# Kernel optimization log

Hardware: AMD Instinct MI355X
Metric: run time of the kernel (lower is better)

The kernel has to match this reference:

```python
import jax, jax.numpy as jnp
import numpy as np

B, NG, H, G, T0, T1 = 4096, 3000, 6, 30, 500, 50  # batch, genes, hidden, genes/term, leaf terms, mid terms
EPS = 1e-5  # BatchNorm1d default eps


def _bn(x, gamma, beta):
    # training-mode BatchNorm1d: biased batch stats over the batch axis
    m = x.mean(axis=0)
    v = ((x - m) ** 2).mean(axis=0)
    return gamma * (x - m) / jnp.sqrt(v + EPS) + beta


def setup_inputs() -> dict:
    key = jax.random.key(0)
    ks = iter(jax.random.split(key, 32))
    rn = lambda shape, s=0.05: jax.random.normal(next(ks), shape, dtype=jnp.float32) * s
    return dict(
        cell_features=jax.random.normal(next(ks), (B, NG), dtype=jnp.float32),
        Wdg=rn((T0 + T1 + 1, G, NG)), bdg=rn((T0 + T1 + 1, G)),
        W0=rn((T0, H, G)), b0=rn((T0, H)), gam0=jnp.ones((T0, H), jnp.float32), bet0=jnp.zeros((T0, H), jnp.float32),
        aw0=rn((T0, H)), ab0=rn((T0,)), av0=rn((T0,)), ac0=rn((T0,)),
        W1=rn((T1, H, 10 * H + G)), b1=rn((T1, H)), gam1=jnp.ones((T1, H), jnp.float32), bet1=jnp.zeros((T1, H), jnp.float32),
        aw1=rn((T1, H)), ab1=rn((T1,)), av1=rn((T1,)), ac1=rn((T1,)),
        W2=rn((H, T1 * H + G)), b2=rn((H,)), gam2=jnp.ones((H,), jnp.float32), bet2=jnp.zeros((H,), jnp.float32),
        aw2=rn((H,)), ab2=rn(()), av2=rn(()), ac2=rn(()),
    )


def reference(cell_features, Wdg, bdg,
              W0, b0, gam0, bet0, aw0, ab0, av0, ac0,
              W1, b1, gam1, bet1, aw1, ab1, av1, ac1,
              W2, b2, gam2, bet2, aw2, ab2, av2, ac2):
    # direct_gene_layer for every term: Linear(ngene -> genes_per_term), no activation
    dg = jnp.einsum('bn,tgn->btg', cell_features, Wdg) + bdg  # [B, 551, G]
    # ---- layer 0 (leaves): input = direct gene output only ----
    z0 = jnp.tanh(jnp.einsum('btg,thg->bth', dg[:, :T0], W0) + b0)
    n0 = _bn(z0, gam0, bet0)                                   # [B, T0, H]
    aux0 = jnp.tanh(jnp.einsum('bth,th->bt', n0, aw0) + ab0) * av0 + ac0
    # ---- layer 1: term t's children are leaves [10t, 10t+10); concat children + direct genes ----
    in1 = jnp.concatenate([n0.reshape(B, T1, 10 * H), dg[:, T0:T0 + T1]], axis=-1)  # [B, T1, 90]
    z1 = jnp.tanh(jnp.einsum('bti,thi->bth', in1, W1) + b1)
    n1 = _bn(z1, gam1, bet1)                                   # [B, T1, H]
    aux1 = jnp.tanh(jnp.einsum('bth,th->bt', n1, aw1) + ab1) * av1 + ac1
    # ---- root: children = all mid terms + direct genes ----
    in2 = jnp.concatenate([n1.reshape(B, T1 * H), dg[:, -1]], axis=-1)  # [B, 330]
    z2 = jnp.tanh(in2 @ W2.T + b2)
    n2 = _bn(z2, gam2, bet2)                                   # [B, H]
    aux2 = jnp.tanh(n2 @ aw2 + ab2) * av2 + ac2                # [B]
    # flatten (aux_out_map, term_NN_out_map) into one array for a single comparable output
    aux_all = jnp.concatenate([aux0, aux1, aux2[:, None]], axis=1)              # [B, 551]
    nn_all = jnp.concatenate([n0.reshape(B, -1), n1.reshape(B, -1), n2], axis=1)  # [B, 551*H]
    return jnp.concatenate([aux_all, nn_all], axis=1)          # [B, 3857]
```

## Files before the change

kernel.cpp:

```cpp
#include <hip/hip_runtime.h>
#include <hip/hip_bf16.h>

#define BATCH 4096
#define NGENE 3000
#define HID   6
#define GPT   30
#define T0N   500
#define T1N   50
#define KP    3008
#define MROWS 4608
#define OUTW  3857
#define BNEPS 1e-5f

typedef __attribute__((ext_vector_type(8))) __bf16 bf16x8;
typedef __attribute__((ext_vector_type(4))) float f32x4;
typedef __attribute__((ext_vector_type(8))) unsigned short ushort8;

__device__ __forceinline__ unsigned short f2bf(float f) {
  unsigned int u = __builtin_bit_cast(unsigned int, f);
  u = (u + 0x7fffu + ((u >> 16) & 1u)) >> 16;
  return (unsigned short)u;
}

__device__ __forceinline__ void gload_lds16(const void* g, void* l) {
  __builtin_amdgcn_global_load_lds(
      (const __attribute__((address_space(1))) unsigned int*)g,
      (__attribute__((address_space(3))) unsigned int*)l, 16, 0, 0);
}

__global__ void cast_cell(const float* __restrict__ x, ushort8* __restrict__ y) {
  int idx = blockIdx.x * 256 + threadIdx.x;
  int r = idx / 376, c8 = idx - r * 376;
  int c = c8 * 8;
  ushort8 o = (ushort8)0;
  if (c < NGENE) {
    const float4* p = (const float4*)(x + (size_t)r * NGENE + c);
    float4 a = p[0], b = p[1];
    o[0] = f2bf(a.x); o[1] = f2bf(a.y); o[2] = f2bf(a.z); o[3] = f2bf(a.w);
    o[4] = f2bf(b.x); o[5] = f2bf(b.y); o[6] = f2bf(b.z); o[7] = f2bf(b.w);
  }
  y[idx] = o;
}

__global__ void v0_build(const float* __restrict__ Wdg, const float* __restrict__ W0,
                         unsigned short* __restrict__ abuf) {
  int n = blockIdx.x * 256 + threadIdx.x;
  int t = blockIdx.y;
  if (n >= KP) return;
  bool valid = n < NGENE;
  float x[GPT];
#pragma unroll
  for (int g = 0; g < GPT; ++g)
    x[g] = valid ? Wdg[((size_t)(t * GPT + g)) * NGENE + n] : 0.f;
#pragma unroll
  for (int h = 0; h < HID; ++h) {
    const float* w = W0 + (t * HID + h) * GPT;
    float s = 0.f;
#pragma unroll
    for (int g = 0; g < GPT; ++g) s += x[g] * w[g];
    abuf[((size_t)(t * HID + h)) * KP + n] = valid ? f2bf(s) : (unsigned short)0;
  }
}

__global__ void cast_wdg_mid(const float* __restrict__ w, ushort8* __restrict__ y) {
  int idx = blockIdx.x * 256 + threadIdx.x;
  if (idx >= 1530 * 376) return;
  int r = idx / 376, c8 = idx - r * 376;
  int c = c8 * 8;
  ushort8 o = (ushort8)0;
  if (c < NGENE) {
    const float4* p = (const float4*)(w + (size_t)(15000 + r) * NGENE + c);
    float4 a = p[0], b = p[1];
    o[0] = f2bf(a.x); o[1] = f2bf(a.y); o[2] = f2bf(a.z); o[3] = f2bf(a.w);
    o[4] = f2bf(b.x); o[5] = f2bf(b.y); o[6] = f2bf(b.z); o[7] = f2bf(b.w);
  }
  y[(size_t)(3000 + r) * 376 + c8] = o;
}

__global__ void zero_tail(ushort8* __restrict__ y) {
  int idx = blockIdx.x * 256 + threadIdx.x;
  if (idx < 78 * 376) y[(size_t)4530 * 376 + idx] = (ushort8)0;
}

__global__ void build_bias(const float* __restrict__ bdg, const float* __restrict__ W0,
                           const float* __restrict__ b0, float* __restrict__ bias) {
  int idx = blockIdx.x * 256 + threadIdx.x;
  if (idx >= MROWS) return;
  float v = 0.f;
  if (idx < 3000) {
    int t = idx / HID;
    float s = b0[idx];
#pragma unroll
    for (int g = 0; g < GPT; ++g) s += W0[idx * GPT + g] * bdg[t * GPT + g];
    v = s;
  } else if (idx < 4530) {
    v = bdg[15000 + idx - 3000];
  }
  bias[idx] = v;
}

__global__ __launch_bounds__(256) void gemm_fused(
    const unsigned short* __restrict__ A,
    const unsigned short* __restrict__ Bt,
    const float* __restrict__ bias,
    float* __restrict__ C) {
  __shared__ unsigned short smem[8192];
  const int tid  = threadIdx.x;
  const int wave = tid >> 6, lane = tid & 63;
  const int wm = wave >> 1, wn = wave & 1;
  const int quad = lane >> 4, fr = lane & 15;
  const int m0 = blockIdx.y * 128, n0 = blockIdx.x * 128;
  const int lrow = lane >> 2;
  const int lcol = (lane & 3) * 8;

  f32x4 acc[16] = {};

  for (int kt = 0; kt < KP / 32; ++kt) {
    const int k0 = kt * 32;
#pragma unroll
    for (int q = 0; q < 4; ++q) {
      int chunk = q * 4 + wave;
      const unsigned short* gsrc;
      if (chunk < 8) {
        int row = m0 + chunk * 16 + lrow;
        gsrc = A + (size_t)row * KP + k0 + lcol;
      } else {
        int row = n0 + (chunk - 8) * 16 + lrow;
        gsrc = Bt + (size_t)row * KP + k0 + lcol;
      }
      gload_lds16(gsrc, &smem[chunk * 512]);
    }
    asm volatile("s_waitcnt vmcnt(0)" ::: "memory");
    __syncthreads();

    bf16x8 af[4], bfr[4];
#pragma unroll
    for (int tm = 0; tm < 4; ++tm)
      af[tm] = ((const bf16x8*)smem)[((wm * 64 + tm * 16 + fr) * 32 + quad * 8) >> 3];
#pragma unroll
    for (int tn = 0; tn < 4; ++tn)
      bfr[tn] = ((const bf16x8*)smem)[(4096 + (wn * 64 + tn * 16 + fr) * 32 + quad * 8) >> 3];
#pragma unroll
    for (int tm = 0; tm < 4; ++tm)
#pragma unroll
      for (int tn = 0; tn < 4; ++tn)
        acc[tm * 4 + tn] = __builtin_amdgcn_mfma_f32_16x16x32_bf16(
            af[tm], bfr[tn], acc[tm * 4 + tn], 0, 0, 0);
    __syncthreads();
  }

#pragma unroll
  for (int tm = 0; tm < 4; ++tm) {
#pragma unroll
    for (int tn = 0; tn < 4; ++tn) {
      int n = n0 + wn * 64 + tn * 16 + fr;
#pragma unroll
      for (int r = 0; r < 4; ++r) {
        int m = m0 + wm * 64 + tm * 16 + quad * 4 + r;
        float v = acc[tm * 4 + tn][r] + bias[m];
        if (m < 3000) v = tanhf(v);
        C[(size_t)m * BATCH + n] = v;
      }
    }
  }
}

__global__ void colstatsT(const float* __restrict__ zT, float* __restrict__ st, int ncols) {
  int c = blockIdx.x;
  if (c >= ncols) return;
  const float* p = zT + (size_t)c * BATCH;
  float s = 0.f, q = 0.f;
  for (int i = threadIdx.x; i < BATCH; i += 256) {
    float v = p[i];
    s += v; q += v * v;
  }
#pragma unroll
  for (int off = 32; off > 0; off >>= 1) {
    s += __shfl_down(s, off);
    q += __shfl_down(q, off);
  }
  __shared__ float ls[8];
  int lane = threadIdx.x & 63, w = threadIdx.x >> 6;
  if (lane == 0) { ls[2 * w] = s; ls[2 * w + 1] = q; }
  __syncthreads();
  if (threadIdx.x == 0) {
    st[2 * c]     = ls[0] + ls[2] + ls[4] + ls[6];
    st[2 * c + 1] = ls[1] + ls[3] + ls[5] + ls[7];
  }
}

__global__ void bnfin(const float* __restrict__ st, const float* __restrict__ gam,
                      const float* __restrict__ bet, float* __restrict__ ss, int ncols) {
  int c = blockIdx.x * 256 + threadIdx.x;
  if (c >= ncols) return;
  float m = st[2 * c] * (1.f / BATCH);
  float v = st[2 * c + 1] * (1.f / BATCH) - m * m;
  float sc = gam[c] * rsqrtf(v + BNEPS);
  ss[2 * c] = sc;
  ss[2 * c + 1] = bet[c] - m * sc;
}

__global__ void norm_emit(const float* __restrict__ zT, const float* __restrict__ ss,
                          float* __restrict__ out, int ncols, int outoff) {
  __shared__ float tile[64][65];
  int lane = threadIdx.x & 63, w = threadIdx.x >> 6;
  int c0 = blockIdx.x * 64, b0 = blockIdx.y * 64;
#pragma unroll
  for (int i = 0; i < 16; ++i) {
    int cc = w * 16 + i, c = c0 + cc;
    float n = 0.f;
    if (c < ncols)
      n = zT[(size_t)c * BATCH + b0 + lane] * ss[2 * c] + ss[2 * c + 1];
    tile[cc][lane] = n;
  }
  __syncthreads();
  int c = c0 + lane;
  if (c < ncols) {
#pragma unroll
    for (int i = 0; i < 16; ++i) {
      int rr = w * 16 + i;
      out[(size_t)(b0 + rr) * OUTW + outoff + c] = tile[lane][rr];
    }
  }
}

__global__ void aux_head(const float* __restrict__ zT, const float* __restrict__ ss,
                         const float* __restrict__ aw, const float* __restrict__ ab,
                         const float* __restrict__ av, const float* __restrict__ ac,
                         float* __restrict__ out, int nterm, int auxoff) {
  int lane = threadIdx.x & 63, tg = threadIdx.x >> 6;
  int t = blockIdx.x * 4 + tg;
  if (t >= nterm) return;
  int b = blockIdx.y * 64 + lane;
  float s = ab[t];
#pragma unroll
  for (int h = 0; h < HID; ++h) {
    int c = t * HID + h;
    float n = zT[(size_t)c * BATCH + b] * ss[2 * c] + ss[2 * c + 1];
    s += n * aw[c];
  }
  out[(size_t)b * OUTW + auxoff + t] = tanhf(s) * av[t] + ac[t];
}

__global__ void layer1_zT(const float* __restrict__ C, const float* __restrict__ ss0,
                          const float* __restrict__ W1, const float* __restrict__ b1,
                          float* __restrict__ z1T, float* __restrict__ st) {
  int lane = threadIdx.x & 63, tg = threadIdx.x >> 6;
  int t = blockIdx.x * 4 + tg;
  if (t >= T1N) return;
  int b = blockIdx.y * 64 + lane;
  const float* z0T = C;
  const float* dgm = C + (size_t)3000 * BATCH;
  float x[90];
#pragma unroll
  for (int j = 0; j < 60; ++j) {
    int c = t * 60 + j;
    x[j] = z0T[(size_t)c * BATCH + b] * ss0[2 * c] + ss0[2 * c + 1];
  }
#pragma unroll
  for (int g = 0; g < GPT; ++g)
    x[60 + g] = dgm[(size_t)(t * GPT + g) * BATCH + b];
#pragma unroll
  for (int h = 0; h < HID; ++h) {
    int c = t * HID + h;
    const float* w = W1 + c * 90;
    float s = b1[c];
#pragma unroll
    for (int i = 0; i < 90; ++i) s += x[i] * w[i];
    float z = tanhf(s);
    z1T[(size_t)c * BATCH + b] = z;
    float s1 = z, s2 = z * z;
#pragma unroll
    for (int off = 32; off > 0; off >>= 1) {
      s1 += __shfl_down(s1, off);
      s2 += __shfl_down(s2, off);
    }
    if (lane == 0) {
      atomicAdd(&st[2 * c], s1);
      atomicAdd(&st[2 * c + 1], s2);
    }
  }
}

__global__ void root_zT(const float* __restrict__ C, const float* __restrict__ z1T,
                        const float* __restrict__ ss1, const float* __restrict__ W2,
                        const float* __restrict__ b2, float* __restrict__ z2T,
                        float* __restrict__ st) {
  int b = blockIdx.x * 256 + threadIdx.x;
  int lane = threadIdx.x & 63;
  const float* dgr = C + (size_t)4500 * BATCH;
  float s[HID];
#pragma unroll
  for (int h = 0; h < HID; ++h) s[h] = b2[h];
  for (int c = 0; c < 300; ++c) {
    float n = z1T[(size_t)c * BATCH + b] * ss1[2 * c] + ss1[2 * c + 1];
#pragma unroll
    for (int h = 0; h < HID; ++h) s[h] += n * W2[h * 330 + c];
  }
#pragma unroll
  for (int g = 0; g < GPT; ++g) {
    float d = dgr[(size_t)g * BATCH + b];
#pragma unroll
    for (int h = 0; h < HID; ++h) s[h] += d * W2[h * 330 + 300 + g];
  }
#pragma unroll
  for (int h = 0; h < HID; ++h) {
    float z = tanhf(s[h]);
    z2T[(size_t)h * BATCH + b] = z;
    float s1 = z, s2 = z * z;
#pragma unroll
    for (int off = 32; off > 0; off >>= 1) {
      s1 += __shfl_down(s1, off);
      s2 += __shfl_down(s2, off);
    }
    if (lane == 0) {
      atomicAdd(&st[2 * h], s1);
      atomicAdd(&st[2 * h + 1], s2);
    }
  }
}

__global__ void root_emit(const float* __restrict__ z2T, const float* __restrict__ ss2,
                          const float* __restrict__ aw2, const float* __restrict__ ab2,
                          const float* __restrict__ av2, const float* __restrict__ ac2,
                          float* __restrict__ out) {
  int b = blockIdx.x * 256 + threadIdx.x;
  float s = ab2[0];
#pragma unroll
  for (int h = 0; h < HID; ++h) {
    float n = z2T[(size_t)h * BATCH + b] * ss2[2 * h] + ss2[2 * h + 1];
    out[(size_t)b * OUTW + 3851 + h] = n;
    s += n * aw2[h];
  }
  out[(size_t)b * OUTW + 550] = tanhf(s) * av2[0] + ac2[0];
}

extern "C" void kernel_launch(void* const* d_in, const int* in_sizes, int n_in,
                              void* d_out, int out_size, void* d_ws, size_t ws_size,
                              hipStream_t stream) {
  (void)in_sizes; (void)n_in; (void)out_size; (void)ws_size;
  const float* cell = (const float*)d_in[0];
  const float* Wdg  = (const float*)d_in[1];
  const float* bdg  = (const float*)d_in[2];
  const float* W0   = (const float*)d_in[3];
  const float* b0   = (const float*)d_in[4];
  const float* gam0 = (const float*)d_in[5];
  const float* bet0 = (const float*)d_in[6];
  const float* aw0  = (const float*)d_in[7];
  const float* ab0  = (const float*)d_in[8];
  const float* av0  = (const float*)d_in[9];
  const float* ac0  = (const float*)d_in[10];
  const float* W1   = (const float*)d_in[11];
  const float* b1   = (const float*)d_in[12];
  const float* gam1 = (const float*)d_in[13];
  const float* bet1 = (const float*)d_in[14];
  const float* aw1  = (const float*)d_in[15];
  const float* ab1  = (const float*)d_in[16];
  const float* av1  = (const float*)d_in[17];
  const float* ac1  = (const float*)d_in[18];
  const float* W2   = (const float*)d_in[19];
  const float* b2   = (const float*)d_in[20];
  const float* gam2 = (const float*)d_in[21];
  const float* bet2 = (const float*)d_in[22];
  const float* aw2  = (const float*)d_in[23];
  const float* ab2  = (const float*)d_in[24];
  const float* av2  = (const float*)d_in[25];
  const float* ac2  = (const float*)d_in[26];
  float* out = (float*)d_out;

  char* ws = (char*)d_ws;
  unsigned short* cellb = (unsigned short*)(ws);
  unsigned short* abuf  = (unsigned short*)(ws + 24641536);
  float*          C     = (float*)(ws + 52363264);
  float*          z1T   = (float*)(ws + 127860736);
  float*          z2T   = (float*)(ws + 132775936);
  float*          st    = (float*)(ws + 132874240);
  float*          ssb   = (float*)(ws + 132907008);
  float*          bias  = (float*)(ws + 132939776);
  float* st0 = st,  *st1 = st + 2 * 3000,  *st2 = st + 2 * 3300;
  float* ss0 = ssb, *ss1 = ssb + 2 * 3000, *ss2 = ssb + 2 * 3300;

  hipMemsetAsync(st, 0, 32768, stream);
  cast_cell<<<6016, 256, 0, stream>>>(cell, (ushort8*)cellb);
  v0_build<<<dim3(12, T0N), 256, 0, stream>>>(Wdg, W0, abuf);
  cast_wdg_mid<<<2248, 256, 0, stream>>>(Wdg, (ushort8*)abuf);
  zero_tail<<<115, 256, 0, stream>>>((ushort8*)abuf);
  build_bias<<<18, 256, 0, stream>>>(bdg, W0, b0, bias);

  gemm_fused<<<dim3(32, 36), 256, 0, stream>>>(abuf, cellb, bias, C);

  colstatsT<<<3000, 256, 0, stream>>>(C, st0, 3000);
  bnfin<<<12, 256, 0, stream>>>(st0, gam0, bet0, ss0, 3000);
  norm_emit<<<dim3(47, 64), 256, 0, stream>>>(C, ss0, out, 3000, 551);
  aux_head<<<dim3(125, 64), 256, 0, stream>>>(C, ss0, aw0, ab0, av0, ac0, out, 500, 0);

  layer1_zT<<<dim3(13, 64), 256, 0, stream>>>(C, ss0, W1, b1, z1T, st1);
  bnfin<<<2, 256, 0, stream>>>(st1, gam1, bet1, ss1, 300);
  norm_emit<<<dim3(5, 64), 256, 0, stream>>>(z1T, ss1, out, 300, 3551);
  aux_head<<<dim3(13, 64), 256, 0, stream>>>(z1T, ss1, aw1, ab1, av1, ac1, out, 50, 500);

  root_zT<<<16, 256, 0, stream>>>(C, z1T, ss1, W2, b2, z2T, st2);
  bnfin<<<1, 256, 0, stream>>>(st2, gam2, bet2, ss2, 6);
  root_emit<<<16, 256, 0, stream>>>(z2T, ss2, aw2, ab2, av2, ac2, out);
}
```

Before: 693.2 us.

## Pipeline GEMM with triple-buffered LDS, fuse BN stats, merge prep and aux kernels

The GEMM moves to 256x128 tiles with 512 threads, triple-buffered LDS prefetch two k-steps ahead, an XOR swizzle for LDS reads, a remapped block order, and s_setprio around the MFMAs. Column sums and sums of squares are now reduced in the GEMM epilogue with atomics, which removes the separate colstats pass over C. The small prep kernels (cast, mid-weight cast, zero tail, bias) are merged into one launch, and norm_emit is fused with aux_head so the tile already in LDS feeds the aux outputs. The trade-offs are atomic contention, different float summation order in the statistics, and higher register and LDS pressure.

```diff
diff --git a/kernel.cpp b/kernel.cpp
--- a/kernel.cpp
+++ b/kernel.cpp
@@ -11,6 +11,8 @@
 #define MROWS 4608
 #define OUTW  3857
 #define BNEPS 1e-5f
+#define NIT   94
+#define BUFU  12288
 
 typedef __attribute__((ext_vector_type(8))) __bf16 bf16x8;
 typedef __attribute__((ext_vector_type(4))) float f32x4;
@@ -28,18 +30,52 @@
       (__attribute__((address_space(3))) unsigned int*)l, 16, 0, 0);
 }
 
-__global__ void cast_cell(const float* __restrict__ x, ushort8* __restrict__ y) {
-  int idx = blockIdx.x * 256 + threadIdx.x;
-  int r = idx / 376, c8 = idx - r * 376;
-  int c = c8 * 8;
-  ushort8 o = (ushort8)0;
-  if (c < NGENE) {
-    const float4* p = (const float4*)(x + (size_t)r * NGENE + c);
-    float4 a = p[0], b = p[1];
-    o[0] = f2bf(a.x); o[1] = f2bf(a.y); o[2] = f2bf(a.z); o[3] = f2bf(a.w);
-    o[4] = f2bf(b.x); o[5] = f2bf(b.y); o[6] = f2bf(b.z); o[7] = f2bf(b.w);
-  }
-  y[idx] = o;
+__global__ void prep(const float* __restrict__ cell, const float* __restrict__ Wdg,
+                     const float* __restrict__ bdg, const float* __restrict__ W0,
+                     const float* __restrict__ b0,
+                     ushort8* __restrict__ cellb, ushort8* __restrict__ abuf8,
+                     float* __restrict__ bias) {
+  int blk = blockIdx.x;
+  if (blk < 6016) {
+    int idx = blk * 256 + threadIdx.x;
+    int r = idx / 376, c8 = idx - r * 376;
+    int c = c8 * 8;
+    ushort8 o = (ushort8)0;
+    if (c < NGENE) {
+      const float4* p = (const float4*)(cell + (size_t)r * NGENE + c);
+      float4 a = p[0], b = p[1];
+      o[0] = f2bf(a.x); o[1] = f2bf(a.y); o[2] = f2bf(a.z); o[3] = f2bf(a.w);
+      o[4] = f2bf(b.x); o[5] = f2bf(b.y); o[6] = f2bf(b.z); o[7] = f2bf(b.w);
+    }
+    cellb[idx] = o;
+  } else if (blk < 8378) {
+    int idx = (blk - 6016) * 256 + threadIdx.x;
+    if (idx >= 1608 * 376) return;
+    int r = idx / 376, c8 = idx - r * 376;
+    int c = c8 * 8;
+    ushort8 o = (ushort8)0;
+    if (r < 1530 && c < NGENE) {
+      const float4* p = (const float4*)(Wdg + (size_t)(15000 + r) * NGENE + c);
+      float4 a = p[0], b = p[1];
+      o[0] = f2bf(a.x); o[1] = f2bf(a.y); o[2] = f2bf(a.z); o[3] = f2bf(a.w);
+      o[4] = f2bf(b.x); o[5] = f2bf(b.y); o[6] = f2bf(b.z); o[7] = f2bf(b.w);
+    }
+    abuf8[(size_t)(3000 + r) * 376 + c8] = o;
+  } else {
+    int idx = (blk - 8378) * 256 + threadIdx.x;
+    if (idx >= MROWS) return;
+    float v = 0.f;
+    if (idx < 3000) {
+      int t = idx / HID;
+      float s = b0[idx];
+#pragma unroll
+      for (int g = 0; g < GPT; ++g) s += W0[idx * GPT + g] * bdg[t * GPT + g];
+      v = s;
+    } else if (idx < 4530) {
+      v = bdg[15000 + idx - 3000];
+    }
+    bias[idx] = v;
+  }
 }
 
 __global__ void v0_build(const float* __restrict__ Wdg, const float* __restrict__ W0,
@@ -62,130 +98,106 @@
   }
 }
 
-__global__ void cast_wdg_mid(const float* __restrict__ w, ushort8* __restrict__ y) {
-  int idx = blockIdx.x * 256 + threadIdx.x;
-  if (idx >= 1530 * 376) return;
-  int r = idx / 376, c8 = idx - r * 376;
-  int c = c8 * 8;
-  ushort8 o = (ushort8)0;
-  if (c < NGENE) {
-    const float4* p = (const float4*)(w + (size_t)(15000 + r) * NGENE + c);
-    float4 a = p[0], b = p[1];
-    o[0] = f2bf(a.x); o[1] = f2bf(a.y); o[2] = f2bf(a.z); o[3] = f2bf(a.w);
-    o[4] = f2bf(b.x); o[5] = f2bf(b.y); o[6] = f2bf(b.z); o[7] = f2bf(b.w);
-  }
-  y[(size_t)(3000 + r) * 376 + c8] = o;
-}
-
-__global__ void zero_tail(ushort8* __restrict__ y) {
-  int idx = blockIdx.x * 256 + threadIdx.x;
-  if (idx < 78 * 376) y[(size_t)4530 * 376 + idx] = (ushort8)0;
-}
-
-__global__ void build_bias(const float* __restrict__ bdg, const float* __restrict__ W0,
-                           const float* __restrict__ b0, float* __restrict__ bias) {
-  int idx = blockIdx.x * 256 + threadIdx.x;
-  if (idx >= MROWS) return;
-  float v = 0.f;
-  if (idx < 3000) {
-    int t = idx / HID;
-    float s = b0[idx];
-#pragma unroll
-    for (int g = 0; g < GPT; ++g) s += W0[idx * GPT + g] * bdg[t * GPT + g];
-    v = s;
-  } else if (idx < 4530) {
-    v = bdg[15000 + idx - 3000];
-  }
-  bias[idx] = v;
-}
-
-__global__ __launch_bounds__(256) void gemm_fused(
+__global__ __launch_bounds__(512, 2) void gemm_fused(
     const unsigned short* __restrict__ A,
     const unsigned short* __restrict__ Bt,
     const float* __restrict__ bias,
-    float* __restrict__ C) {
-  __shared__ unsigned short smem[8192];
+    float* __restrict__ C,
+    float* __restrict__ st) {
+  extern __shared__ unsigned short smem[];
   const int tid  = threadIdx.x;
   const int wave = tid >> 6, lane = tid & 63;
   const int wm = wave >> 1, wn = wave & 1;
   const int quad = lane >> 4, fr = lane & 15;
-  const int m0 = blockIdx.y * 128, n0 = blockIdx.x * 128;
-  const int lrow = lane >> 2;
-  const int lcol = (lane & 3) * 8;
-
-  f32x4 acc[16] = {};
-
-  for (int kt = 0; kt < KP / 32; ++kt) {
-    const int k0 = kt * 32;
-#pragma unroll
-    for (int q = 0; q < 4; ++q) {
-      int chunk = q * 4 + wave;
-      const unsigned short* gsrc;
-      if (chunk < 8) {
-        int row = m0 + chunk * 16 + lrow;
-        gsrc = A + (size_t)row * KP + k0 + lcol;
-      } else {
-        int row = n0 + (chunk - 8) * 16 + lrow;
-        gsrc = Bt + (size_t)row * KP + k0 + lcol;
+
+  const int bid = blockIdx.x;
+  const int wg  = (bid & 7) * 72 + (bid >> 3);
+  const int m0 = (wg >> 5) * 256;
+  const int n0 = (wg & 31) * 128;
+
+  const int r   = tid >> 2;
+  const int ssw = (tid & 3) ^ ((r >> 2) & 3);
+  const unsigned short* gA0 = A  + (size_t)(m0 + r) * KP + ssw * 8;
+  const unsigned short* gA1 = A  + (size_t)(m0 + 128 + r) * KP + ssw * 8;
+  const unsigned short* gB0 = Bt + (size_t)(n0 + r) * KP + ssw * 8;
+  const int dA0 = wave * 512;
+  const int dA1 = 4096 + wave * 512;
+  const int dB0 = 8192 + wave * 512;
+
+  f32x4 acc[4][4] = {};
+
+#pragma unroll
+  for (int t = 0; t < 2; ++t) {
+    unsigned short* base = smem + t * BUFU;
+    gload_lds16(gA0 + t * 32, base + dA0);
+    gload_lds16(gA1 + t * 32, base + dA1);
+    gload_lds16(gB0 + t * 32, base + dB0);
+  }
+  asm volatile("s_waitcnt vmcnt(3)" ::: "memory");
+  __builtin_amdgcn_s_barrier();
+
+  const int swz  = (quad ^ ((fr >> 2) & 3)) << 3;
+  const int aoff = (wm * 64 + fr) * 32 + swz;
+  const int boff = 8192 + (wn * 64 + fr) * 32 + swz;
+
+  int cur = 0;
+  for (int t = 0; t < NIT; ++t) {
+    if (t < NIT - 2) {
+      unsigned short* sb = smem + ((cur >= 1) ? cur - 1 : 2) * BUFU;
+      const int ko = (t + 2) * 32;
+      gload_lds16(gA0 + ko, sb + dA0);
+      gload_lds16(gA1 + ko, sb + dA1);
+      gload_lds16(gB0 + ko, sb + dB0);
+    }
+    const unsigned short* buf = smem + cur * BUFU;
+    bf16x8 af[4], bf[4];
+#pragma unroll
+    for (int i = 0; i < 4; ++i) af[i] = *(const bf16x8*)(buf + aoff + i * 512);
+#pragma unroll
+    for (int j = 0; j < 4; ++j) bf[j] = *(const bf16x8*)(buf + boff + j * 512);
+    __builtin_amdgcn_s_setprio(1);
+#pragma unroll
+    for (int i = 0; i < 4; ++i)
+#pragma unroll
+      for (int j = 0; j < 4; ++j)
+        acc[i][j] = __builtin_amdgcn_mfma_f32_16x16x32_bf16(af[i], bf[j], acc[i][j], 0, 0, 0);
+    __builtin_amdgcn_s_setprio(0);
+    asm volatile("s_waitcnt lgkmcnt(0)" ::: "memory");
+    if (t < NIT - 2) asm volatile("s_waitcnt vmcnt(3)" ::: "memory");
+    else             asm volatile("s_waitcnt vmcnt(0)" ::: "memory");
+    __builtin_amdgcn_s_barrier();
+    cur = (cur == 2) ? 0 : cur + 1;
+  }
+
+  const int mbase = m0 + wm * 64 + quad * 4;
+  const int nbase = n0 + wn * 64 + fr;
+#pragma unroll
+  for (int i = 0; i < 4; ++i) {
+#pragma unroll
+    for (int rr = 0; rr < 4; ++rr) {
+      const int m = mbase + i * 16 + rr;
+      const float bia = bias[m];
+      const bool act = m < 3000;
+      float s = 0.f, q = 0.f;
+#pragma unroll
+      for (int j = 0; j < 4; ++j) {
+        float v = acc[i][j][rr] + bia;
+        if (act) v = tanhf(v);
+        C[(size_t)m * BATCH + nbase + j * 16] = v;
+        s += v; q += v * v;
       }
-      gload_lds16(gsrc, &smem[chunk * 512]);
-    }
-    asm volatile("s_waitcnt vmcnt(0)" ::: "memory");
-    __syncthreads();
-
-    bf16x8 af[4], bfr[4];
-#pragma unroll
-    for (int tm = 0; tm < 4; ++tm)
-      af[tm] = ((const bf16x8*)smem)[((wm * 64 + tm * 16 + fr) * 32 + quad * 8) >> 3];
-#pragma unroll
-    for (int tn = 0; tn < 4; ++tn)
-      bfr[tn] = ((const bf16x8*)smem)[(4096 + (wn * 64 + tn * 16 + fr) * 32 + quad * 8) >> 3];
-#pragma unroll
-    for (int tm = 0; tm < 4; ++tm)
-#pragma unroll
-      for (int tn = 0; tn < 4; ++tn)
-        acc[tm * 4 + tn] = __builtin_amdgcn_mfma_f32_16x16x32_bf16(
-            af[tm], bfr[tn], acc[tm * 4 + tn], 0, 0, 0);
-    __syncthreads();
-  }
-
-#pragma unroll
-  for (int tm = 0; tm < 4; ++tm) {
-#pragma unroll
-    for (int tn = 0; tn < 4; ++tn) {
-      int n = n0 + wn * 64 + tn * 16 + fr;
-#pragma unroll
-      for (int r = 0; r < 4; ++r) {
-        int m = m0 + wm * 64 + tm * 16 + quad * 4 + r;
-        float v = acc[tm * 4 + tn][r] + bias[m];
-        if (m < 3000) v = tanhf(v);
-        C[(size_t)m * BATCH + n] = v;
+      if (act) {
+#pragma unroll
+        for (int off = 1; off < 16; off <<= 1) {
+          s += __shfl_xor(s, off);
+          q += __shfl_xor(q, off);
+        }
+        if (fr == 0) {
+          atomicAdd(&st[2 * m], s);
+          atomicAdd(&st[2 * m + 1], q);
+        }
       }
     }
-  }
-}
-
-__global__ void colstatsT(const float* __restrict__ zT, float* __restrict__ st, int ncols) {
-  int c = blockIdx.x;
-  if (c >= ncols) return;
-  const float* p = zT + (size_t)c * BATCH;
-  float s = 0.f, q = 0.f;
-  for (int i = threadIdx.x; i < BATCH; i += 256) {
-    float v = p[i];
-    s += v; q += v * v;
-  }
-#pragma unroll
-  for (int off = 32; off > 0; off >>= 1) {
-    s += __shfl_down(s, off);
-    q += __shfl_down(q, off);
-  }
-  __shared__ float ls[8];
-  int lane = threadIdx.x & 63, w = threadIdx.x >> 6;
-  if (lane == 0) { ls[2 * w] = s; ls[2 * w + 1] = q; }
-  __syncthreads();
-  if (threadIdx.x == 0) {
-    st[2 * c]     = ls[0] + ls[2] + ls[4] + ls[6];
-    st[2 * c + 1] = ls[1] + ls[3] + ls[5] + ls[7];
   }
 }
 
@@ -200,46 +212,42 @@
   ss[2 * c + 1] = bet[c] - m * sc;
 }
 
-__global__ void norm_emit(const float* __restrict__ zT, const float* __restrict__ ss,
-                          float* __restrict__ out, int ncols, int outoff) {
-  __shared__ float tile[64][65];
+__global__ void norm_emit_aux(const float* __restrict__ zT, const float* __restrict__ ss,
+                              const float* __restrict__ aw, const float* __restrict__ ab,
+                              const float* __restrict__ av, const float* __restrict__ ac,
+                              float* __restrict__ out, int ncols, int outoff,
+                              int auxoff, int nterm) {
+  __shared__ float tile[66][65];
   int lane = threadIdx.x & 63, w = threadIdx.x >> 6;
-  int c0 = blockIdx.x * 64, b0 = blockIdx.y * 64;
-#pragma unroll
-  for (int i = 0; i < 16; ++i) {
-    int cc = w * 16 + i, c = c0 + cc;
+  int c0 = blockIdx.x * 66, b0 = blockIdx.y * 64;
+  for (int cc = w; cc < 66; cc += 4) {
+    int c = c0 + cc;
     float n = 0.f;
     if (c < ncols)
       n = zT[(size_t)c * BATCH + b0 + lane] * ss[2 * c] + ss[2 * c + 1];
     tile[cc][lane] = n;
   }
   __syncthreads();
-  int c = c0 + lane;
-  if (c < ncols) {
-#pragma unroll
-    for (int i = 0; i < 16; ++i) {
-      int rr = w * 16 + i;
-      out[(size_t)(b0 + rr) * OUTW + outoff + c] = tile[lane][rr];
-    }
-  }
-}
-
-__global__ void aux_head(const float* __restrict__ zT, const float* __restrict__ ss,
-                         const float* __restrict__ aw, const float* __restrict__ ab,
-                         const float* __restrict__ av, const float* __restrict__ ac,
-                         float* __restrict__ out, int nterm, int auxoff) {
-  int lane = threadIdx.x & 63, tg = threadIdx.x >> 6;
-  int t = blockIdx.x * 4 + tg;
-  if (t >= nterm) return;
-  int b = blockIdx.y * 64 + lane;
-  float s = ab[t];
-#pragma unroll
-  for (int h = 0; h < HID; ++h) {
-    int c = t * HID + h;
-    float n = zT[(size_t)c * BATCH + b] * ss[2 * c] + ss[2 * c + 1];
-    s += n * aw[c];
-  }
-  out[(size_t)b * OUTW + auxoff + t] = tanhf(s) * av[t] + ac[t];
+  for (int cl = lane; cl < 66; cl += 64) {
+    int c = c0 + cl;
+    if (c < ncols) {
+#pragma unroll
+      for (int i = 0; i < 16; ++i) {
+        int rr = w * 16 + i;
+        out[(size_t)(b0 + rr) * OUTW + outoff + c] = tile[cl][rr];
+      }
+    }
+  }
+  int t0 = c0 / 6;
+  for (int tl = w; tl < 11; tl += 4) {
+    int t = t0 + tl;
+    if (t < nterm && c0 + tl * 6 < ncols) {
+      float s = ab[t];
+#pragma unroll
+      for (int h = 0; h < HID; ++h) s += tile[tl * 6 + h][lane] * aw[t * HID + h];
+      out[(size_t)(b0 + lane) * OUTW + auxoff + t] = tanhf(s) * av[t] + ac[t];
+    }
+  }
 }
 
 __global__ void layer1_zT(const float* __restrict__ C, const float* __restrict__ ss0,
@@ -380,24 +388,28 @@
   float* st0 = st,  *st1 = st + 2 * 3000,  *st2 = st + 2 * 3300;
   float* ss0 = ssb, *ss1 = ssb + 2 * 3000, *ss2 = ssb + 2 * 3300;
 
+  static int s_attr = 0;
+  if (!s_attr) {
+    hipFuncSetAttribute(reinterpret_cast<const void*>(gemm_fused),
+                        hipFuncAttributeMaxDynamicSharedMemorySize, 73728);
+    s_attr = 1;
+  }
+
   hipMemsetAsync(st, 0, 32768, stream);
-  cast_cell<<<6016, 256, 0, stream>>>(cell, (ushort8*)cellb);
+  prep<<<8396, 256, 0, stream>>>(cell, Wdg, bdg, W0, b0,
+                                 (ushort8*)cellb, (ushort8*)abuf, bias);
   v0_build<<<dim3(12, T0N), 256, 0, stream>>>(Wdg, W0, abuf);
-  cast_wdg_mid<<<2248, 256, 0, stream>>>(Wdg, (ushort8*)abuf);
-  zero_tail<<<115, 256, 0, stream>>>((ushort8*)abuf);
-  build_bias<<<18, 256, 0, stream>>>(bdg, W0, b0, bias);
-
-  gemm_fused<<<dim3(32, 36), 256, 0, stream>>>(abuf, cellb, bias, C);
-
-  colstatsT<<<3000, 256, 0, stream>>>(C, st0, 3000);
+
+  gemm_fused<<<576, 512, 73728, stream>>>(abuf, cellb, bias, C, st0);
+
   bnfin<<<12, 256, 0, stream>>>(st0, gam0, bet0, ss0, 3000);
-  norm_emit<<<dim3(47, 64), 256, 0, stream>>>(C, ss0, out, 3000, 551);
-  aux_head<<<dim3(125, 64), 256, 0, stream>>>(C, ss0, aw0, ab0, av0, ac0, out, 500, 0);
+  norm_emit_aux<<<dim3(46, 64), 256, 0, stream>>>(C, ss0, aw0, ab0, av0, ac0,
+                                                  out, 3000, 551, 0, 500);
 
   layer1_zT<<<dim3(13, 64), 256, 0, stream>>>(C, ss0, W1, b1, z1T, st1);
   bnfin<<<2, 256, 0, stream>>>(st1, gam1, bet1, ss1, 300);
-  norm_emit<<<dim3(5, 64), 256, 0, stream>>>(z1T, ss1, out, 300, 3551);
-  aux_head<<<dim3(13, 64), 256, 0, stream>>>(z1T, ss1, aw1, ab1, av1, ac1, out, 50, 500);
+  norm_emit_aux<<<dim3(5, 64), 256, 0, stream>>>(z1T, ss1, aw1, ab1, av1, ac1,
+                                                 out, 300, 3551, 500, 50);
 
   root_zT<<<16, 256, 0, stream>>>(C, z1T, ss1, W2, b2, z2T, st2);
   bnfin<<<1, 256, 0, stream>>>(st2, gam2, bet2, ss2, 6);
```

Result: faster. 678.5 us (-2.1%).
